# Performance work log

Measured on AMD Instinct MI355X. Metric: run time of the kernel, lower is better.

The kernel has to match this reference:

```python
import jax, jax.numpy as jnp
import numpy as np

EPS = 1e-5
KH = KW = 3
PAD = 1

def conv3x3(x, w, b=None):
    out = jax.lax.conv_general_dilated(
        x, w, window_strides=(1, 1), padding=((PAD, PAD), (PAD, PAD)),
        dimension_numbers=("NCHW", "OIHW", "NCHW"))
    if b is not None:
        out = out + b[None, :, None, None]
    return out

def batchnorm(x, gamma, beta):
    # training-mode BatchNorm2d: batch statistics over (N, H, W)
    mean = x.mean(axis=(0, 2, 3), keepdims=True)
    var = x.var(axis=(0, 2, 3), keepdims=True)
    return gamma[None, :, None, None] * (x - mean) / jnp.sqrt(var + EPS) + beta[None, :, None, None]

def bilinear_gather(x, y_pos, x_pos):
    # x: [B,C,H,W]; y_pos/x_pos: [B,P,H,W] (P = KH*KW sampling taps)
    # zero padding outside image (mmcv modulated deform conv semantics)
    B, C, H, W = x.shape
    P = y_pos.shape[1]
    x_flat = x.reshape(B, C, H * W)
    y0 = jnp.floor(y_pos)
    x0 = jnp.floor(x_pos)
    ly = y_pos - y0
    lx = x_pos - x0
    out = jnp.zeros((B, C, P, H, W), dtype=x.dtype)
    for dy, dx, wgt in ((0, 0, (1 - ly) * (1 - lx)), (0, 1, (1 - ly) * lx),
                        (1, 0, ly * (1 - lx)), (1, 1, ly * lx)):
        yi = y0 + dy
        xi = x0 + dx
        valid = ((yi >= 0) & (yi <= H - 1) & (xi >= 0) & (xi <= W - 1)).astype(x.dtype)
        yc = jnp.clip(yi, 0, H - 1).astype(jnp.int32)
        xc = jnp.clip(xi, 0, W - 1).astype(jnp.int32)
        idx = (yc * W + xc).reshape(B, 1, P * H * W)
        vals = jnp.take_along_axis(x_flat, jnp.broadcast_to(idx, (B, C, P * H * W)), axis=2)
        vals = vals.reshape(B, C, P, H, W)
        out = out + vals * (wgt * valid)[:, None]
    return out  # [B,C,P,H,W]

def modulated_deform_conv(x, w_off, b_off, w_dcn):
    B, C, H, W = x.shape
    P = KH * KW
    off = conv3x3(x, w_off, b_off)  # [B, 3*P, H, W]
    o1, o2, m = jnp.split(off, 3, axis=1)
    offset = jnp.concatenate([o1, o2], axis=1)            # [B, 2P, H, W]
    offset = offset.reshape(B, P, 2, H, W)                # channel 2p -> dy, 2p+1 -> dx
    mask = jax.nn.sigmoid(m)                              # [B, P, H, W]
    hh = jnp.arange(H, dtype=x.dtype)
    ww = jnp.arange(W, dtype=x.dtype)
    ky = jnp.arange(KH, dtype=x.dtype)
    kx = jnp.arange(KW, dtype=x.dtype)
    # base sampling grid per tap p = ky*KW + kx: (h - PAD + ky, w - PAD + kx)
    base_y = (hh[None, :] - PAD + ky[:, None])            # [KH, H]
    base_x = (ww[None, :] - PAD + kx[:, None])            # [KW, W]
    base_y = jnp.broadcast_to(base_y[:, None, :, None], (KH, KW, H, W)).reshape(P, H, W)
    base_x = jnp.broadcast_to(base_x[None, :, None, :], (KH, KW, H, W)).reshape(P, H, W)
    y_pos = base_y[None] + offset[:, :, 0]                # [B,P,H,W]
    x_pos = base_x[None] + offset[:, :, 1]
    sampled = bilinear_gather(x, y_pos, x_pos)            # [B,C,P,H,W]
    sampled = sampled * mask[:, None]
    w = w_dcn.reshape(w_dcn.shape[0], C, P)               # [O, C, P]
    return jnp.einsum("bcphw,ocp->bohw", sampled, w)

def setup_inputs() -> dict:
    key = jax.random.key(0)
    ks = jax.random.split(key, 10)
    B, Ch, H, W = 4, 256, 64, 64
    Cin, Cout = 2 * Ch, 256
    P = KH * KW
    inp = {
        "input_v": jax.random.normal(ks[0], (B, Ch, H, W), jnp.float32),
        "input_i": jax.random.normal(ks[1], (B, Ch, H, W), jnp.float32),
        "w_off": jax.random.normal(ks[2], (3 * P, Cin, KH, KW), jnp.float32) * 0.01,
        "b_off": jnp.zeros((3 * P,), jnp.float32),
        "w_dcn": jax.random.normal(ks[3], (Cout, Cin, KH, KW), jnp.float32) * (1.0 / np.sqrt(Cin * P)),
        "gamma1": jnp.ones((Cout,), jnp.float32),
        "beta1": jnp.zeros((Cout,), jnp.float32),
        "w2": jax.random.normal(ks[4], (Cout, Cout, KH, KW), jnp.float32) * (1.0 / np.sqrt(Cout * P)),
        "gamma2": jnp.ones((Cout,), jnp.float32),
        "beta2": jnp.zeros((Cout,), jnp.float32),
    }
    return inp

def reference(input_v, input_i, w_off, b_off, w_dcn, gamma1, beta1, w2, gamma2, beta2):
    x = jnp.concatenate([input_v, input_i], axis=1)
    out = modulated_deform_conv(x, w_off, b_off, w_dcn)
    out = jax.nn.relu(batchnorm(out, gamma1, beta1))
    out = jax.nn.relu(batchnorm(conv3x3(out, w2), gamma2, beta2))
    return out
```

## Files before the change

kernel.cpp:

```cpp
#include <hip/hip_runtime.h>
#include <cstdint>
#include <cstddef>

typedef unsigned short u16;
typedef __attribute__((ext_vector_type(8))) short s16x8;
typedef __attribute__((ext_vector_type(4))) float f32x4;

#define DEV __device__ __forceinline__

DEV float bf2f(short u){
  union { unsigned int i; float f; } v;
  v.i = ((unsigned int)(u16)u) << 16;
  return v.f;
}
DEV short f2bf(float f){
  union { float f; unsigned int i; } v; v.f = f;
  unsigned int u = v.i;
  u += 0x7fffu + ((u >> 16) & 1u);
  return (short)(u >> 16);
}
DEV s16x8 s16x8_zero(){
  s16x8 z;
#pragma unroll
  for(int j=0;j<8;j++) z[j]=0;
  return z;
}
DEV f32x4 f32x4_zero(){
  f32x4 z;
#pragma unroll
  for(int j=0;j<4;j++) z[j]=0.f;
  return z;
}
DEV f32x4 mfma16(s16x8 a, s16x8 b, f32x4 c){
  return __builtin_amdgcn_mfma_f32_16x16x32_bf16(a, b, c, 0, 0, 0);
}

static constexpr size_t OFF_ACC_B  = 0;
static constexpr size_t OUT1_ACC_B = 2097152;
static constexpr size_t OUT2_ACC_B = OUT1_ACC_B + 16777216;
static constexpr size_t STATS_B    = OUT2_ACC_B + 16777216;
static constexpr size_t ZERO_BYTES = STATS_B + 4096;
static constexpr size_t XN_B       = ZERO_BYTES;
static constexpr size_t OUT1N_B    = XN_B + 16777216;
static constexpr size_t WOFFT_B    = OUT1N_B + 8388608;
static constexpr size_t WDCNT_B    = WOFFT_B + 294912;
static constexpr size_t W2T_B      = WDCNT_B + 2359296;

__global__ void k_x_to_nhwc(const float* __restrict__ v, const float* __restrict__ vi,
                            u16* __restrict__ xn){
  __shared__ float tile[64][65];
  const int b = blockIdx.z, c0 = blockIdx.y*64, hw0 = blockIdx.x*64;
  const float* src = (c0 < 256) ? (v  + ((size_t)b*256 + c0)      *4096)
                                : (vi + ((size_t)b*256 + (c0-256))*4096);
  const int t = threadIdx.x;
#pragma unroll
  for(int k=0;k<16;k++){
    int idx = t + k*256;
    int cl = idx >> 6, wl = idx & 63;
    tile[cl][wl] = src[(size_t)cl*4096 + hw0 + wl];
  }
  __syncthreads();
#pragma unroll
  for(int k=0;k<16;k++){
    int idx = t + k*256;
    int wl = idx >> 6, cl = idx & 63;
    xn[(size_t)(b*4096 + hw0 + wl)*512 + c0 + cl] = (u16)f2bf(tile[cl][wl]);
  }
}

__global__ void k_prep_woff(const float* __restrict__ w, u16* __restrict__ wt){
  int idx = blockIdx.x*256 + threadIdx.x;
  if(idx >= 32*4608) return;
  int n = idx / 4608, k = idx % 4608;
  int t = k >> 9, c = k & 511;
  float val = (n < 27) ? w[(size_t)(n*512 + c)*9 + t] : 0.f;
  wt[idx] = (u16)f2bf(val);
}
__global__ void k_prep_wdcn(const float* __restrict__ w, u16* __restrict__ wt){
  int idx = blockIdx.x*256 + threadIdx.x;
  if(idx >= 256*4608) return;
  int n = idx / 4608, k = idx % 4608;
  int t = k >> 9, c = k & 511;
  wt[idx] = (u16)f2bf(w[(size_t)(n*512 + c)*9 + t]);
}
__global__ void k_prep_w2(const float* __restrict__ w, u16* __restrict__ wt){
  int idx = blockIdx.x*256 + threadIdx.x;
  if(idx >= 256*2304) return;
  int n = idx / 2304, k = idx % 2304;
  int t = k >> 8, c = k & 255;
  wt[idx] = (u16)f2bf(w[(size_t)(n*256 + c)*9 + t]);
}

__global__ __launch_bounds__(256, 4) void k_conv_off(
    const u16* __restrict__ xn, const u16* __restrict__ wt, float* __restrict__ offa){
  __shared__ short A_lds[4][128][8];
  __shared__ short B_lds[4][32][8];
  const int tid = threadIdx.x;
  const int lane = tid & 63, wid = tid >> 6;
  const int quad = lane >> 4, ln = lane & 15;
  const int m0 = blockIdx.x * 128;
  const int b = m0 >> 12;
  const int h0 = (m0 & 4095) >> 6;
  const int ks = blockIdx.y >> 1;
  const int chh = blockIdx.y & 1;
  const int CH0 = chh << 8;
  const int ts0 = (ks == 3) ? 6 : ks*2;
  const int ntap = (ks == 3) ? 3 : 2;
  const int m_base = wid * 32;
  const int r = tid >> 1, sp = (tid & 1) * 2;
  const int h_r = h0 + (r >> 6), w_r = r & 63;
  const s16x8* Ap = (const s16x8*)A_lds;
  const s16x8* Bp = (const s16x8*)B_lds;
  f32x4 acc[2][2];
#pragma unroll
  for(int mf=0;mf<2;mf++)
#pragma unroll
    for(int nf=0;nf<2;nf++) acc[mf][nf] = f32x4_zero();

  s16x8 v0, v1, bv;
  auto load_it = [&](int it){
    const int tp = ts0 + (it >> 3);
    const int ty = tp/3, tx = tp - ty*3;
    const int y = h_r - 1 + ty, x = w_r - 1 + tx;
    const bool vld = (y>=0) & (y<64) & (x>=0) & (x<64);
    const int cA = CH0 + (it & 7)*32;
    v0 = s16x8_zero(); v1 = s16x8_zero();
    if(vld){
      const u16* src = xn + ((size_t)((b<<12) + (y<<6) + x) << 9) + cA + sp*8;
      v0 = *(const s16x8*)(src);
      v1 = *(const s16x8*)(src + 8);
    }
    if(tid < 128){
      const int n = tid & 31, s2 = tid >> 5;
      bv = *(const s16x8*)(wt + (size_t)n*4608 + tp*512 + cA + s2*8);
    }
  };

  const int NIT = ntap * 8;
  load_it(0);
  for(int it = 0; it < NIT; ++it){
    __syncthreads();
    *(s16x8*)(&A_lds[sp][r][0])   = v0;
    *(s16x8*)(&A_lds[sp+1][r][0]) = v1;
    if(tid < 128){
      const int n = tid & 31, s2 = tid >> 5;
      *(s16x8*)(&B_lds[s2][n][0]) = bv;
    }
    if(it + 1 < NIT) load_it(it + 1);
    __syncthreads();
    s16x8 a0 = Ap[quad*128 + m_base + ln];
    s16x8 a1 = Ap[quad*128 + m_base + 16 + ln];
    s16x8 b0 = Bp[quad*32 + ln];
    s16x8 b1 = Bp[quad*32 + 16 + ln];
    acc[0][0] = mfma16(a0, b0, acc[0][0]);
    acc[0][1] = mfma16(a0, b1, acc[0][1]);
    acc[1][0] = mfma16(a1, b0, acc[1][0]);
    acc[1][1] = mfma16(a1, b1, acc[1][1]);
  }
#pragma unroll
  for(int mf=0;mf<2;mf++)
#pragma unroll
    for(int nf=0;nf<2;nf++){
      const int col = nf*16 + ln;
#pragma unroll
      for(int i=0;i<4;i++){
        const int row = m_base + mf*16 + quad*4 + i;
        unsafeAtomicAdd(offa + (size_t)(m0+row)*32 + col, acc[mf][nf][i]);
      }
    }
}

__global__ __launch_bounds__(256, 4) void k_dcn(
    const u16* __restrict__ xn, const u16* __restrict__ wt,
    const float* __restrict__ offa, const float* __restrict__ boff,
    float* __restrict__ outa){
  __shared__ short A_lds[4][64][8];
  __shared__ short B_lds[4][256][8];
  __shared__ int   p_ofs[5][4][64];
  __shared__ float p_wgt[5][4][64];
  const int tid = threadIdx.x;
  const int lane = tid & 63, wid = tid >> 6;
  const int quad = lane >> 4, ln = lane & 15;
  const int m0 = blockIdx.x * 64;
  const int b = m0 >> 12;
  const int h = (m0 & 4095) >> 6;
  const int tg = blockIdx.y >> 1;
  const int chh = blockIdx.y & 1;
  const int CH0 = chh << 8;
  const int ts0 = tg ? 4 : 0;
  const int ntap = tg ? 5 : 4;
  const int wm = wid >> 1, wn = wid & 1;
  const int m_base = wm*32, n_base = wn*128;
  const int r = tid >> 2, sub = tid & 3;
  const s16x8* Ap = (const s16x8*)A_lds;
  const s16x8* Bp = (const s16x8*)B_lds;
  const u16* wrowt = wt + (size_t)tid*4608;
  f32x4 acc[2][8];
#pragma unroll
  for(int mf=0;mf<2;mf++)
#pragma unroll
    for(int nf=0;nf<8;nf++) acc[mf][nf] = f32x4_zero();

  {
    const int rr = tid & 63;
    const float* orow = offa + (size_t)(m0+rr)*32;
    for(int tpi = tid >> 6; tpi < ntap; tpi += 4){
      const int tp = ts0 + tpi;
      float dy = orow[2*tp]   + boff[2*tp];
      float dx = orow[2*tp+1] + boff[2*tp+1];
      float mz = orow[18+tp]  + boff[18+tp];
      float mk = 1.f / (1.f + expf(-mz));
      float ypos = (float)(h - 1 + tp/3) + dy;
      float xpos = (float)(rr - 1 + tp%3) + dx;
      float y0f = floorf(ypos), x0f = floorf(xpos);
      float ly = ypos - y0f, lx = xpos - x0f;
      int y0 = (int)y0f, x0 = (int)x0f;
#pragma unroll
      for(int k=0;k<4;k++){
        int ddy = k >> 1, ddx = k & 1;
        int yi = y0 + ddy, xi = x0 + ddx;
        bool vv = (yi >= 0) & (yi < 64) & (xi >= 0) & (xi < 64);
        float wk = (ddy ? ly : 1.f-ly) * (ddx ? lx : 1.f-lx) * mk;
        if(!vv) wk = 0.f;
        int yc = yi < 0 ? 0 : (yi > 63 ? 63 : yi);
        int xc = xi < 0 ? 0 : (xi > 63 ? 63 : xi);
        p_ofs[tpi][k][rr] = ((b << 12) + (yc << 6) + xc) << 9;
        p_wgt[tpi][k][rr] = wk;
      }
    }
  }
  __syncthreads();

  s16x8 a0, a1, a2, a3, b0, b1, b2, b3;
  float w0, w1, w2, w3;
  auto loadA = [&](int it){
    const int tpi = it >> 3;
    const int c0 = CH0 + (it & 7)*32 + sub*8;
    w0 = p_wgt[tpi][0][r]; w1 = p_wgt[tpi][1][r];
    w2 = p_wgt[tpi][2][r]; w3 = p_wgt[tpi][3][r];
    a0 = *(const s16x8*)(xn + p_ofs[tpi][0][r] + c0);
    a1 = *(const s16x8*)(xn + p_ofs[tpi][1][r] + c0);
    a2 = *(const s16x8*)(xn + p_ofs[tpi][2][r] + c0);
    a3 = *(const s16x8*)(xn + p_ofs[tpi][3][r] + c0);
  };
  auto loadB = [&](int it){
    const int kb = (ts0 + (it >> 3))*512 + CH0 + (it & 7)*32;
    b0 = *(const s16x8*)(wrowt + kb);
    b1 = *(const s16x8*)(wrowt + kb + 8);
    b2 = *(const s16x8*)(wrowt + kb + 16);
    b3 = *(const s16x8*)(wrowt + kb + 24);
  };

  const int NIT = ntap * 8;
  loadA(0); loadB(0);
  for(int it = 0; it < NIT; ++it){
    s16x8 pk;
#pragma unroll
    for(int j=0;j<8;j++){
      float f = w0 * bf2f(a0[j]);
      f = fmaf(w1, bf2f(a1[j]), f);
      f = fmaf(w2, bf2f(a2[j]), f);
      f = fmaf(w3, bf2f(a3[j]), f);
      pk[j] = f2bf(f);
    }
    const bool more = (it + 1 < NIT);
    if(more) loadA(it + 1);
    __syncthreads();
    *(s16x8*)(&A_lds[sub][r][0]) = pk;
    *(s16x8*)(&B_lds[0][tid][0]) = b0;
    *(s16x8*)(&B_lds[1][tid][0]) = b1;
    *(s16x8*)(&B_lds[2][tid][0]) = b2;
    *(s16x8*)(&B_lds[3][tid][0]) = b3;
    if(more) loadB(it + 1);
    __syncthreads();
    s16x8 af0 = Ap[quad*64 + m_base + ln];
    s16x8 af1 = Ap[quad*64 + m_base + 16 + ln];
    s16x8 bfr[8];
#pragma unroll
    for(int nf=0;nf<8;nf++) bfr[nf] = Bp[quad*256 + n_base + nf*16 + ln];
#pragma unroll
    for(int nf=0;nf<8;nf++){
      acc[0][nf] = mfma16(af0, bfr[nf], acc[0][nf]);
      acc[1][nf] = mfma16(af1, bfr[nf], acc[1][nf]);
    }
  }
#pragma unroll
  for(int mf=0;mf<2;mf++)
#pragma unroll
    for(int nf=0;nf<8;nf++){
      const int col = n_base + nf*16 + ln;
#pragma unroll
      for(int i=0;i<4;i++){
        const int row = m_base + mf*16 + quad*4 + i;
        unsafeAtomicAdd(outa + (size_t)(m0+row)*256 + col, acc[mf][nf][i]);
      }
    }
}

__global__ __launch_bounds__(256, 4) void k_conv2(
    const u16* __restrict__ a_in, const u16* __restrict__ wt, float* __restrict__ outa){
  __shared__ short A_lds[4][64][8];
  __shared__ short B_lds[4][256][8];
  const int tid = threadIdx.x;
  const int lane = tid & 63, wid = tid >> 6;
  const int quad = lane >> 4, ln = lane & 15;
  const int m0 = blockIdx.x * 64;
  const int b = m0 >> 12;
  const int h = (m0 & 4095) >> 6;
  const int tg = blockIdx.y >> 1;
  const int chh = blockIdx.y & 1;
  const int CH0 = chh << 7;
  const int ts0 = tg ? 4 : 0;
  const int ntap = tg ? 5 : 4;
  const int wm = wid >> 1, wn = wid & 1;
  const int m_base = wm*32, n_base = wn*128;
  const int r = tid >> 2, sub = tid & 3;
  const s16x8* Ap = (const s16x8*)A_lds;
  const s16x8* Bp = (const s16x8*)B_lds;
  const u16* wrowt = wt + (size_t)tid*2304;
  f32x4 acc[2][8];
#pragma unroll
  for(int mf=0;mf<2;mf++)
#pragma unroll
    for(int nf=0;nf<8;nf++) acc[mf][nf] = f32x4_zero();

  s16x8 va, b0, b1, b2, b3;
  auto load_it = [&](int it){
    const int tp = ts0 + (it >> 2);
    const int ty = tp/3, tx = tp - ty*3;
    const int y = h - 1 + ty, x = r - 1 + tx;
    const bool vld = (y>=0) & (y<64) & (x>=0) & (x<64);
    const int c0 = CH0 + (it & 3)*32;
    va = s16x8_zero();
    if(vld) va = *(const s16x8*)(a_in + (((size_t)((b<<12) + (y<<6) + x)) << 8) + c0 + sub*8);
    const int kb = tp*256 + c0;
    b0 = *(const s16x8*)(wrowt + kb);
    b1 = *(const s16x8*)(wrowt + kb + 8);
    b2 = *(const s16x8*)(wrowt + kb + 16);
    b3 = *(const s16x8*)(wrowt + kb + 24);
  };

  const int NIT = ntap * 4;
  load_it(0);
  for(int it = 0; it < NIT; ++it){
    __syncthreads();
    *(s16x8*)(&A_lds[sub][r][0]) = va;
    *(s16x8*)(&B_lds[0][tid][0]) = b0;
    *(s16x8*)(&B_lds[1][tid][0]) = b1;
    *(s16x8*)(&B_lds[2][tid][0]) = b2;
    *(s16x8*)(&B_lds[3][tid][0]) = b3;
    if(it + 1 < NIT) load_it(it + 1);
    __syncthreads();
    s16x8 af0 = Ap[quad*64 + m_base + ln];
    s16x8 af1 = Ap[quad*64 + m_base + 16 + ln];
    s16x8 bfr[8];
#pragma unroll
    for(int nf=0;nf<8;nf++) bfr[nf] = Bp[quad*256 + n_base + nf*16 + ln];
#pragma unroll
    for(int nf=0;nf<8;nf++){
      acc[0][nf] = mfma16(af0, bfr[nf], acc[0][nf]);
      acc[1][nf] = mfma16(af1, bfr[nf], acc[1][nf]);
    }
  }
#pragma unroll
  for(int mf=0;mf<2;mf++)
#pragma unroll
    for(int nf=0;nf<8;nf++){
      const int col = n_base + nf*16 + ln;
#pragma unroll
      for(int i=0;i<4;i++){
        const int row = m_base + mf*16 + quad*4 + i;
        unsafeAtomicAdd(outa + (size_t)(m0+row)*256 + col, acc[mf][nf][i]);
      }
    }
}

__global__ void k_stats(const float* __restrict__ acc, float* __restrict__ sum,
                        float* __restrict__ sq){
  const int m0 = blockIdx.x*64;
  const int c = threadIdx.x;
  float s = 0.f, q = 0.f;
  for(int i=0;i<64;i++){
    float v = acc[(size_t)(m0+i)*256 + c];
    s += v; q += v*v;
  }
  unsafeAtomicAdd(sum + c, s);
  unsafeAtomicAdd(sq + c, q);
}

__global__ void k_bn1(const float* __restrict__ acc, const float* __restrict__ sum,
                      const float* __restrict__ sq, const float* __restrict__ g,
                      const float* __restrict__ bt, u16* __restrict__ o){
  __shared__ float sc[256], sh[256];
  const int t = threadIdx.x;
  {
    float mean = sum[t] * (1.f/16384.f);
    float var  = sq[t] * (1.f/16384.f) - mean*mean;
    float rstd = rsqrtf(var + 1e-5f);
    float s = g[t] * rstd;
    sc[t] = s; sh[t] = bt[t] - mean*s;
  }
  __syncthreads();
  const int c4 = (t & 63) * 4;
  const float s0 = sc[c4], s1 = sc[c4+1], s2 = sc[c4+2], s3 = sc[c4+3];
  const float h0 = sh[c4], h1 = sh[c4+1], h2 = sh[c4+2], h3 = sh[c4+3];
#pragma unroll
  for(int k=0;k<4;k++){
    int m = blockIdx.x*16 + k*4 + (t>>6);
    const float4 v = *(const float4*)(acc + (size_t)m*256 + c4);
    unsigned int lo = (unsigned int)(u16)f2bf(fmaxf(0.f, v.x*s0 + h0))
                    | ((unsigned int)(u16)f2bf(fmaxf(0.f, v.y*s1 + h1)) << 16);
    unsigned int hi = (unsigned int)(u16)f2bf(fmaxf(0.f, v.z*s2 + h2))
                    | ((unsigned int)(u16)f2bf(fmaxf(0.f, v.w*s3 + h3)) << 16);
    uint2 pr; pr.x = lo; pr.y = hi;
    *(uint2*)(o + (size_t)m*256 + c4) = pr;
  }
}

__global__ void k_bn2_out(const float* __restrict__ acc, const float* __restrict__ sum,
                          const float* __restrict__ sq, const float* __restrict__ g,
                          const float* __restrict__ bt, float* __restrict__ out){
  __shared__ float tile[64][65];
  __shared__ float sc[64], sh[64];
  const int t = threadIdx.x;
  const int b = blockIdx.z, c0 = blockIdx.y*64, hw0 = blockIdx.x*64;
  if(t < 64){
    int c = c0 + t;
    float mean = sum[c] * (1.f/16384.f);
    float var  = sq[c] * (1.f/16384.f) - mean*mean;
    float rstd = rsqrtf(var + 1e-5f);
    float s = g[c] * rstd;
    sc[t] = s; sh[t] = bt[c] - mean*s;
  }
  __syncthreads();
#pragma unroll
  for(int k=0;k<16;k++){
    int idx = t + k*256;
    int wl = idx >> 6, cl = idx & 63;
    float v = acc[(size_t)((b<<12) + hw0 + wl)*256 + c0 + cl];
    tile[wl][cl] = fmaxf(0.f, v*sc[cl] + sh[cl]);
  }
  __syncthreads();
#pragma unroll
  for(int k=0;k<16;k++){
    int idx = t + k*256;
    int cl = idx >> 6, wl = idx & 63;
    out[(size_t)(b*256 + c0 + cl)*4096 + hw0 + wl] = tile[wl][cl];
  }
}

extern "C" void kernel_launch(void* const* d_in, const int* in_sizes, int n_in,
                              void* d_out, int out_size, void* d_ws, size_t ws_size,
                              hipStream_t stream){
  const float* in_v  = (const float*)d_in[0];
  const float* in_i  = (const float*)d_in[1];
  const float* w_off = (const float*)d_in[2];
  const float* b_off = (const float*)d_in[3];
  const float* w_dcn = (const float*)d_in[4];
  const float* g1    = (const float*)d_in[5];
  const float* bt1   = (const float*)d_in[6];
  const float* w2    = (const float*)d_in[7];
  const float* g2    = (const float*)d_in[8];
  const float* bt2   = (const float*)d_in[9];
  float* out = (float*)d_out;
  char* ws = (char*)d_ws;

  float* off_acc  = (float*)(ws + OFF_ACC_B);
  float* out1_acc = (float*)(ws + OUT1_ACC_B);
  float* out2_acc = (float*)(ws + OUT2_ACC_B);
  float* stats    = (float*)(ws + STATS_B);
  float* sum1 = stats,       *sq1 = stats + 256;
  float* sum2 = stats + 512, *sq2 = stats + 768;
  u16* xn    = (u16*)(ws + XN_B);
  u16* out1n = (u16*)(ws + OUT1N_B);
  u16* wofft = (u16*)(ws + WOFFT_B);
  u16* wdcnt = (u16*)(ws + WDCNT_B);
  u16* w2t   = (u16*)(ws + W2T_B);

  hipMemsetAsync(ws, 0, ZERO_BYTES, stream);
  k_x_to_nhwc<<<dim3(64,8,4), 256, 0, stream>>>(in_v, in_i, xn);
  k_prep_woff<<<576, 256, 0, stream>>>(w_off, wofft);
  k_prep_wdcn<<<4608, 256, 0, stream>>>(w_dcn, wdcnt);
  k_prep_w2<<<2304, 256, 0, stream>>>(w2, w2t);
  k_conv_off<<<dim3(128,8), 256, 0, stream>>>(xn, wofft, off_acc);
  k_dcn<<<dim3(256,4), 256, 0, stream>>>(xn, wdcnt, off_acc, b_off, out1_acc);
  k_stats<<<256, 256, 0, stream>>>(out1_acc, sum1, sq1);
  k_bn1<<<1024, 256, 0, stream>>>(out1_acc, sum1, sq1, g1, bt1, out1n);
  k_conv2<<<dim3(256,4), 256, 0, stream>>>(out1n, w2t, out2_acc);
  k_stats<<<256, 256, 0, stream>>>(out2_acc, sum2, sq2);
  k_bn2_out<<<dim3(64,4,4), 256, 0, stream>>>(out2_acc, sum2, sq2, g2, bt2, out);
}
```

Measured before the change: 396.9 us.

## Drop channel split-K and double-buffer register prefetch in conv GEMM kernels

Removes the channel-half split along grid y in the offset conv, deformable conv and second conv, so each block now covers all input channels and issues half as many atomic accumulations into the fp32 output buffers. The main loops are unrolled by two with two register sets of prefetched operands, loading two iterations ahead to hide global-load latency. Launch bounds drop from 4 to 2 blocks per SM to leave room for the extra registers. The trade-off is half as many blocks in flight and longer per-block serial loops, which may reduce occupancy and latency hiding.

```diff
diff --git a/kernel.cpp b/kernel.cpp
--- a/kernel.cpp
+++ b/kernel.cpp
@@ -91,7 +91,7 @@
   wt[idx] = (u16)f2bf(w[(size_t)(n*256 + c)*9 + t]);
 }
 
-__global__ __launch_bounds__(256, 4) void k_conv_off(
+__global__ __launch_bounds__(256, 2) void k_conv_off(
     const u16* __restrict__ xn, const u16* __restrict__ wt, float* __restrict__ offa){
   __shared__ short A_lds[4][128][8];
   __shared__ short B_lds[4][32][8];
@@ -101,9 +101,7 @@
   const int m0 = blockIdx.x * 128;
   const int b = m0 >> 12;
   const int h0 = (m0 & 4095) >> 6;
-  const int ks = blockIdx.y >> 1;
-  const int chh = blockIdx.y & 1;
-  const int CH0 = chh << 8;
+  const int ks = blockIdx.y;
   const int ts0 = (ks == 3) ? 6 : ks*2;
   const int ntap = (ks == 3) ? 3 : 2;
   const int m_base = wid * 32;
@@ -117,13 +115,12 @@
 #pragma unroll
     for(int nf=0;nf<2;nf++) acc[mf][nf] = f32x4_zero();
 
-  s16x8 v0, v1, bv;
-  auto load_it = [&](int it){
-    const int tp = ts0 + (it >> 3);
+  auto load_it = [&](int it, s16x8& v0, s16x8& v1, s16x8& bv){
+    const int tp = ts0 + (it >> 4);
+    const int cA = (it & 15)*32;
     const int ty = tp/3, tx = tp - ty*3;
     const int y = h_r - 1 + ty, x = w_r - 1 + tx;
     const bool vld = (y>=0) & (y<64) & (x>=0) & (x<64);
-    const int cA = CH0 + (it & 7)*32;
     v0 = s16x8_zero(); v1 = s16x8_zero();
     if(vld){
       const u16* src = xn + ((size_t)((b<<12) + (y<<6) + x) << 9) + cA + sp*8;
@@ -136,26 +133,50 @@
     }
   };
 
-  const int NIT = ntap * 8;
-  load_it(0);
-  for(int it = 0; it < NIT; ++it){
-    __syncthreads();
-    *(s16x8*)(&A_lds[sp][r][0])   = v0;
-    *(s16x8*)(&A_lds[sp+1][r][0]) = v1;
+  const int NIT = ntap * 16;
+  s16x8 v0a, v1a, bva, v0b, v1b, bvb;
+  bva = s16x8_zero(); bvb = s16x8_zero();
+  load_it(0, v0a, v1a, bva);
+  load_it(1, v0b, v1b, bvb);
+  for(int it = 0; it < NIT; it += 2){
+    __syncthreads();
+    *(s16x8*)(&A_lds[sp][r][0])   = v0a;
+    *(s16x8*)(&A_lds[sp+1][r][0]) = v1a;
     if(tid < 128){
       const int n = tid & 31, s2 = tid >> 5;
-      *(s16x8*)(&B_lds[s2][n][0]) = bv;
-    }
-    if(it + 1 < NIT) load_it(it + 1);
-    __syncthreads();
-    s16x8 a0 = Ap[quad*128 + m_base + ln];
-    s16x8 a1 = Ap[quad*128 + m_base + 16 + ln];
-    s16x8 b0 = Bp[quad*32 + ln];
-    s16x8 b1 = Bp[quad*32 + 16 + ln];
-    acc[0][0] = mfma16(a0, b0, acc[0][0]);
-    acc[0][1] = mfma16(a0, b1, acc[0][1]);
-    acc[1][0] = mfma16(a1, b0, acc[1][0]);
-    acc[1][1] = mfma16(a1, b1, acc[1][1]);
+      *(s16x8*)(&B_lds[s2][n][0]) = bva;
+    }
+    if(it + 2 < NIT) load_it(it + 2, v0a, v1a, bva);
+    __syncthreads();
+    {
+      s16x8 a0 = Ap[quad*128 + m_base + ln];
+      s16x8 a1 = Ap[quad*128 + m_base + 16 + ln];
+      s16x8 b0 = Bp[quad*32 + ln];
+      s16x8 b1 = Bp[quad*32 + 16 + ln];
+      acc[0][0] = mfma16(a0, b0, acc[0][0]);
+      acc[0][1] = mfma16(a0, b1, acc[0][1]);
+      acc[1][0] = mfma16(a1, b0, acc[1][0]);
+      acc[1][1] = mfma16(a1, b1, acc[1][1]);
+    }
+    __syncthreads();
+    *(s16x8*)(&A_lds[sp][r][0])   = v0b;
+    *(s16x8*)(&A_lds[sp+1][r][0]) = v1b;
+    if(tid < 128){
+      const int n = tid & 31, s2 = tid >> 5;
+      *(s16x8*)(&B_lds[s2][n][0]) = bvb;
+    }
+    if(it + 3 < NIT) load_it(it + 3, v0b, v1b, bvb);
+    __syncthreads();
+    {
+      s16x8 a0 = Ap[quad*128 + m_base + ln];
+      s16x8 a1 = Ap[quad*128 + m_base + 16 + ln];
+      s16x8 b0 = Bp[quad*32 + ln];
+      s16x8 b1 = Bp[quad*32 + 16 + ln];
+      acc[0][0] = mfma16(a0, b0, acc[0][0]);
+      acc[0][1] = mfma16(a0, b1, acc[0][1]);
+      acc[1][0] = mfma16(a1, b0, acc[1][0]);
+      acc[1][1] = mfma16(a1, b1, acc[1][1]);
+    }
   }
 #pragma unroll
   for(int mf=0;mf<2;mf++)
@@ -170,7 +191,7 @@
     }
 }
 
-__global__ __launch_bounds__(256, 4) void k_dcn(
+__global__ __launch_bounds__(256, 2) void k_dcn(
     const u16* __restrict__ xn, const u16* __restrict__ wt,
     const float* __restrict__ offa, const float* __restrict__ boff,
     float* __restrict__ outa){
@@ -184,9 +205,7 @@
   const int m0 = blockIdx.x * 64;
   const int b = m0 >> 12;
   const int h = (m0 & 4095) >> 6;
-  const int tg = blockIdx.y >> 1;
-  const int chh = blockIdx.y & 1;
-  const int CH0 = chh << 8;
+  const int tg = blockIdx.y;
   const int ts0 = tg ? 4 : 0;
   const int ntap = tg ? 5 : 4;
   const int wm = wid >> 1, wn = wid & 1;
@@ -231,11 +250,10 @@
   }
   __syncthreads();
 
-  s16x8 a0, a1, a2, a3, b0, b1, b2, b3;
-  float w0, w1, w2, w3;
-  auto loadA = [&](int it){
-    const int tpi = it >> 3;
-    const int c0 = CH0 + (it & 7)*32 + sub*8;
+  auto loadA = [&](int it, s16x8& a0, s16x8& a1, s16x8& a2, s16x8& a3,
+                   float& w0, float& w1, float& w2, float& w3){
+    const int tpi = it >> 4;
+    const int c0 = (it & 15)*32 + sub*8;
     w0 = p_wgt[tpi][0][r]; w1 = p_wgt[tpi][1][r];
     w2 = p_wgt[tpi][2][r]; w3 = p_wgt[tpi][3][r];
     a0 = *(const s16x8*)(xn + p_ofs[tpi][0][r] + c0);
@@ -243,17 +261,15 @@
     a2 = *(const s16x8*)(xn + p_ofs[tpi][2][r] + c0);
     a3 = *(const s16x8*)(xn + p_ofs[tpi][3][r] + c0);
   };
-  auto loadB = [&](int it){
-    const int kb = (ts0 + (it >> 3))*512 + CH0 + (it & 7)*32;
+  auto loadB = [&](int it, s16x8& b0, s16x8& b1, s16x8& b2, s16x8& b3){
+    const int kb = (ts0 + (it >> 4))*512 + (it & 15)*32;
     b0 = *(const s16x8*)(wrowt + kb);
     b1 = *(const s16x8*)(wrowt + kb + 8);
     b2 = *(const s16x8*)(wrowt + kb + 16);
     b3 = *(const s16x8*)(wrowt + kb + 24);
   };
-
-  const int NIT = ntap * 8;
-  loadA(0); loadB(0);
-  for(int it = 0; it < NIT; ++it){
+  auto blend = [&](const s16x8& a0, const s16x8& a1, const s16x8& a2, const s16x8& a3,
+                   float w0, float w1, float w2, float w3){
     s16x8 pk;
 #pragma unroll
     for(int j=0;j<8;j++){
@@ -263,25 +279,62 @@
       f = fmaf(w3, bf2f(a3[j]), f);
       pk[j] = f2bf(f);
     }
-    const bool more = (it + 1 < NIT);
-    if(more) loadA(it + 1);
-    __syncthreads();
-    *(s16x8*)(&A_lds[sub][r][0]) = pk;
-    *(s16x8*)(&B_lds[0][tid][0]) = b0;
-    *(s16x8*)(&B_lds[1][tid][0]) = b1;
-    *(s16x8*)(&B_lds[2][tid][0]) = b2;
-    *(s16x8*)(&B_lds[3][tid][0]) = b3;
-    if(more) loadB(it + 1);
-    __syncthreads();
-    s16x8 af0 = Ap[quad*64 + m_base + ln];
-    s16x8 af1 = Ap[quad*64 + m_base + 16 + ln];
-    s16x8 bfr[8];
-#pragma unroll
-    for(int nf=0;nf<8;nf++) bfr[nf] = Bp[quad*256 + n_base + nf*16 + ln];
-#pragma unroll
-    for(int nf=0;nf<8;nf++){
-      acc[0][nf] = mfma16(af0, bfr[nf], acc[0][nf]);
-      acc[1][nf] = mfma16(af1, bfr[nf], acc[1][nf]);
+    return pk;
+  };
+
+  const int NIT = ntap * 16;
+  s16x8 aA0,aA1,aA2,aA3, bA0,bA1,bA2,bA3;
+  s16x8 aB0,aB1,aB2,aB3, bB0,bB1,bB2,bB3;
+  float wA0,wA1,wA2,wA3, wB0,wB1,wB2,wB3;
+  loadA(0, aA0,aA1,aA2,aA3, wA0,wA1,wA2,wA3);
+  loadB(0, bA0,bA1,bA2,bA3);
+  loadA(1, aB0,aB1,aB2,aB3, wB0,wB1,wB2,wB3);
+  loadB(1, bB0,bB1,bB2,bB3);
+
+  for(int it = 0; it < NIT; it += 2){
+    {
+      s16x8 pk = blend(aA0,aA1,aA2,aA3, wA0,wA1,wA2,wA3);
+      if(it + 2 < NIT) loadA(it + 2, aA0,aA1,aA2,aA3, wA0,wA1,wA2,wA3);
+      __syncthreads();
+      *(s16x8*)(&A_lds[sub][r][0]) = pk;
+      *(s16x8*)(&B_lds[0][tid][0]) = bA0;
+      *(s16x8*)(&B_lds[1][tid][0]) = bA1;
+      *(s16x8*)(&B_lds[2][tid][0]) = bA2;
+      *(s16x8*)(&B_lds[3][tid][0]) = bA3;
+      if(it + 2 < NIT) loadB(it + 2, bA0,bA1,bA2,bA3);
+      __syncthreads();
+      s16x8 af0 = Ap[quad*64 + m_base + ln];
+      s16x8 af1 = Ap[quad*64 + m_base + 16 + ln];
+      s16x8 bfr[8];
+#pragma unroll
+      for(int nf=0;nf<8;nf++) bfr[nf] = Bp[quad*256 + n_base + nf*16 + ln];
+#pragma unroll
+      for(int nf=0;nf<8;nf++){
+        acc[0][nf] = mfma16(af0, bfr[nf], acc[0][nf]);
+        acc[1][nf] = mfma16(af1, bfr[nf], acc[1][nf]);
+      }
+    }
+    {
+      s16x8 pk = blend(aB0,aB1,aB2,aB3, wB0,wB1,wB2,wB3);
+      if(it + 3 < NIT) loadA(it + 3, aB0,aB1,aB2,aB3, wB0,wB1,wB2,wB3);
+      __syncthreads();
+      *(s16x8*)(&A_lds[sub][r][0]) = pk;
+      *(s16x8*)(&B_lds[0][tid][0]) = bB0;
+      *(s16x8*)(&B_lds[1][tid][0]) = bB1;
+      *(s16x8*)(&B_lds[2][tid][0]) = bB2;
+      *(s16x8*)(&B_lds[3][tid][0]) = bB3;
+      if(it + 3 < NIT) loadB(it + 3, bB0,bB1,bB2,bB3);
+      __syncthreads();
+      s16x8 af0 = Ap[quad*64 + m_base + ln];
+      s16x8 af1 = Ap[quad*64 + m_base + 16 + ln];
+      s16x8 bfr[8];
+#pragma unroll
+      for(int nf=0;nf<8;nf++) bfr[nf] = Bp[quad*256 + n_base + nf*16 + ln];
+#pragma unroll
+      for(int nf=0;nf<8;nf++){
+        acc[0][nf] = mfma16(af0, bfr[nf], acc[0][nf]);
+        acc[1][nf] = mfma16(af1, bfr[nf], acc[1][nf]);
+      }
     }
   }
 #pragma unroll
@@ -297,7 +350,7 @@
     }
 }
 
-__global__ __launch_bounds__(256, 4) void k_conv2(
+__global__ __launch_bounds__(256, 2) void k_conv2(
     const u16* __restrict__ a_in, const u16* __restrict__ wt, float* __restrict__ outa){
   __shared__ short A_lds[4][64][8];
   __shared__ short B_lds[4][256][8];
@@ -307,9 +360,7 @@
   const int m0 = blockIdx.x * 64;
   const int b = m0 >> 12;
   const int h = (m0 & 4095) >> 6;
-  const int tg = blockIdx.y >> 1;
-  const int chh = blockIdx.y & 1;
-  const int CH0 = chh << 7;
+  const int tg = blockIdx.y;
   const int ts0 = tg ? 4 : 0;
   const int ntap = tg ? 5 : 4;
   const int wm = wid >> 1, wn = wid & 1;
@@ -324,13 +375,12 @@
 #pragma unroll
     for(int nf=0;nf<8;nf++) acc[mf][nf] = f32x4_zero();
 
-  s16x8 va, b0, b1, b2, b3;
-  auto load_it = [&](int it){
-    const int tp = ts0 + (it >> 2);
+  auto load_it = [&](int it, s16x8& va, s16x8& b0, s16x8& b1, s16x8& b2, s16x8& b3){
+    const int tp = ts0 + (it >> 3);
+    const int c0 = (it & 7)*32;
     const int ty = tp/3, tx = tp - ty*3;
     const int y = h - 1 + ty, x = r - 1 + tx;
     const bool vld = (y>=0) & (y<64) & (x>=0) & (x<64);
-    const int c0 = CH0 + (it & 3)*32;
     va = s16x8_zero();
     if(vld) va = *(const s16x8*)(a_in + (((size_t)((b<<12) + (y<<6) + x)) << 8) + c0 + sub*8);
     const int kb = tp*256 + c0;
@@ -340,26 +390,51 @@
     b3 = *(const s16x8*)(wrowt + kb + 24);
   };
 
-  const int NIT = ntap * 4;
-  load_it(0);
-  for(int it = 0; it < NIT; ++it){
-    __syncthreads();
-    *(s16x8*)(&A_lds[sub][r][0]) = va;
-    *(s16x8*)(&B_lds[0][tid][0]) = b0;
-    *(s16x8*)(&B_lds[1][tid][0]) = b1;
-    *(s16x8*)(&B_lds[2][tid][0]) = b2;
-    *(s16x8*)(&B_lds[3][tid][0]) = b3;
-    if(it + 1 < NIT) load_it(it + 1);
-    __syncthreads();
-    s16x8 af0 = Ap[quad*64 + m_base + ln];
-    s16x8 af1 = Ap[quad*64 + m_base + 16 + ln];
-    s16x8 bfr[8];
-#pragma unroll
-    for(int nf=0;nf<8;nf++) bfr[nf] = Bp[quad*256 + n_base + nf*16 + ln];
-#pragma unroll
-    for(int nf=0;nf<8;nf++){
-      acc[0][nf] = mfma16(af0, bfr[nf], acc[0][nf]);
-      acc[1][nf] = mfma16(af1, bfr[nf], acc[1][nf]);
+  const int NIT = ntap * 8;
+  s16x8 vA, bA0,bA1,bA2,bA3;
+  s16x8 vB, bB0,bB1,bB2,bB3;
+  load_it(0, vA, bA0,bA1,bA2,bA3);
+  load_it(1, vB, bB0,bB1,bB2,bB3);
+  for(int it = 0; it < NIT; it += 2){
+    __syncthreads();
+    *(s16x8*)(&A_lds[sub][r][0]) = vA;
+    *(s16x8*)(&B_lds[0][tid][0]) = bA0;
+    *(s16x8*)(&B_lds[1][tid][0]) = bA1;
+    *(s16x8*)(&B_lds[2][tid][0]) = bA2;
+    *(s16x8*)(&B_lds[3][tid][0]) = bA3;
+    if(it + 2 < NIT) load_it(it + 2, vA, bA0,bA1,bA2,bA3);
+    __syncthreads();
+    {
+      s16x8 af0 = Ap[quad*64 + m_base + ln];
+      s16x8 af1 = Ap[quad*64 + m_base + 16 + ln];
+      s16x8 bfr[8];
+#pragma unroll
+      for(int nf=0;nf<8;nf++) bfr[nf] = Bp[quad*256 + n_base + nf*16 + ln];
+#pragma unroll
+      for(int nf=0;nf<8;nf++){
+        acc[0][nf] = mfma16(af0, bfr[nf], acc[0][nf]);
+        acc[1][nf] = mfma16(af1, bfr[nf], acc[1][nf]);
+      }
+    }
+    __syncthreads();
+    *(s16x8*)(&A_lds[sub][r][0]) = vB;
+    *(s16x8*)(&B_lds[0][tid][0]) = bB0;
+    *(s16x8*)(&B_lds[1][tid][0]) = bB1;
+    *(s16x8*)(&B_lds[2][tid][0]) = bB2;
+    *(s16x8*)(&B_lds[3][tid][0]) = bB3;
+    if(it + 3 < NIT) load_it(it + 3, vB, bB0,bB1,bB2,bB3);
+    __syncthreads();
+    {
+      s16x8 af0 = Ap[quad*64 + m_base + ln];
+      s16x8 af1 = Ap[quad*64 + m_base + 16 + ln];
+      s16x8 bfr[8];
+#pragma unroll
+      for(int nf=0;nf<8;nf++) bfr[nf] = Bp[quad*256 + n_base + nf*16 + ln];
+#pragma unroll
+      for(int nf=0;nf<8;nf++){
+        acc[0][nf] = mfma16(af0, bfr[nf], acc[0][nf]);
+        acc[1][nf] = mfma16(af1, bfr[nf], acc[1][nf]);
+      }
     }
   }
 #pragma unroll
@@ -482,11 +557,11 @@
   k_prep_woff<<<576, 256, 0, stream>>>(w_off, wofft);
   k_prep_wdcn<<<4608, 256, 0, stream>>>(w_dcn, wdcnt);
   k_prep_w2<<<2304, 256, 0, stream>>>(w2, w2t);
-  k_conv_off<<<dim3(128,8), 256, 0, stream>>>(xn, wofft, off_acc);
-  k_dcn<<<dim3(256,4), 256, 0, stream>>>(xn, wdcnt, off_acc, b_off, out1_acc);
+  k_conv_off<<<dim3(128,4), 256, 0, stream>>>(xn, wofft, off_acc);
+  k_dcn<<<dim3(256,2), 256, 0, stream>>>(xn, wdcnt, off_acc, b_off, out1_acc);
   k_stats<<<256, 256, 0, stream>>>(out1_acc, sum1, sq1);
   k_bn1<<<1024, 256, 0, stream>>>(out1_acc, sum1, sq1, g1, bt1, out1n);
-  k_conv2<<<dim3(256,4), 256, 0, stream>>>(out1n, w2t, out2_acc);
+  k_conv2<<<dim3(256,2), 256, 0, stream>>>(out1n, w2t, out2_acc);
   k_stats<<<256, 256, 0, stream>>>(out2_acc, sum2, sq2);
   k_bn2_out<<<dim3(64,4,4), 256, 0, stream>>>(out2_acc, sum2, sq2, g2, bt2, out);
 }
```

Measured after the change: 352.7 us. -11.2%, faster.
